# Kernel optimization log

Hardware: AMD Instinct MI355X
Metric: run time of the kernel (lower is better)

The kernel has to match this reference:

```python
import jax, jax.numpy as jnp
import numpy as np

H, W = 480, 640
OFFSETS = (1, 3, 5)
AXES = ('ud', 'lr', 'lu', 'ld')
EPS = 1e-18

def _xy_homo():
    yy, xx = jnp.meshgrid(jnp.arange(H, dtype=jnp.float32),
                          jnp.arange(W, dtype=jnp.float32), indexing='ij')
    return jnp.stack([xx.reshape(-1), yy.reshape(-1),
                      jnp.ones(H * W, jnp.float32)], 0)  # [3, H*W]

def _denom(normal, K_inv, xyh, dx, dy):
    # plane-induced denominator with pixel grid shifted by (dx, dy)
    b, _, h, w = normal.shape
    off = jnp.array([dx, dy, 0.0], jnp.float32)[:, None]
    p = jnp.matmul(K_inv, xyh + off).reshape(b, 3, h, w)
    return jnp.sum(normal * p, axis=1, keepdims=True)

def _shift_zero(t, o, axis):
    # zero-filled shifted copies per the torch cat patterns (conf / rgb)
    b, c, h, w = t.shape
    z = lambda *s: jnp.zeros((b, c) + s, t.dtype)
    cat = jnp.concatenate
    if axis == 'ud':
        return (cat([z(o, w), t[:, :, :-o, :]], 2),
                cat([t[:, :, o:, :], z(o, w)], 2))
    if axis == 'lr':
        return (cat([z(h, o), t[:, :, :, :-o]], 3),
                cat([t[:, :, :, o:], z(h, o)], 3))
    if axis == 'lu':
        t1 = cat([z(o, w), cat([z(h - o, o), t[:, :, :-o, :-o]], 3)], 2)
        t2 = cat([cat([t[:, :, o:, o:], z(h - o, o)], 3), z(o, w)], 2)
        return t1, t2
    # ld
    t1 = cat([cat([z(o, w - o), t[:, :, :-o, o:]], 2), z(h, o)], 3)
    t2 = cat([z(h, o), cat([t[:, :, o:, :-o], z(o, w - o)], 2)], 3)
    return t1, t2

def _propagate_axis(depth, normal, rgb, conf, o, K_inv, xyh, nom, axis):
    cat = jnp.concatenate
    def dprop(dx, dy):
        den = _denom(normal, K_inv, xyh, dx, dy)
        return jnp.clip(nom / (den + EPS), 0.01, 10.0)
    if axis == 'ud':
        d1 = cat([depth[:, :, :o, :], dprop(0, o)[:, :, :-o, :]], 2)
        d2 = cat([dprop(0, -o)[:, :, o:, :], depth[:, :, -o:, :]], 2)
    elif axis == 'lr':
        d1 = cat([depth[:, :, :, :o], dprop(o, 0)[:, :, :, :-o]], 3)
        d2 = cat([dprop(-o, 0)[:, :, :, o:], depth[:, :, :, -o:]], 3)
    elif axis == 'lu':
        d1t = cat([depth[:, :, o:, :o], dprop(o, o)[:, :, :-o, :-o]], 3)
        d1 = cat([depth[:, :, :o, :], d1t], 2)
        d2t = cat([dprop(-o, -o)[:, :, o:, o:], depth[:, :, :-o, -o:]], 3)
        d2 = cat([d2t, depth[:, :, -o:, :]], 2)
    else:  # 'ld'
        d1t = cat([depth[:, :, :o, :-o], dprop(-o, o)[:, :, :-o, o:]], 2)
        d1 = cat([d1t, depth[:, :, :, -o:]], 3)
        d2t = cat([dprop(o, -o)[:, :, o:, :-o], depth[:, :, -o:, :-o]], 2)
        d2 = cat([depth[:, :, :, :o], d2t], 3)
    conf1, conf2 = _shift_zero(conf, o, axis)
    rgb1, rgb2 = _shift_zero(rgb, o, axis)
    return d1, d2, conf1, conf2, rgb1, rgb2

def setup_inputs() -> dict:
    key = jax.random.key(0)
    k1, k2, k3, k4 = jax.random.split(key, 4)
    b = 2
    depth = jax.random.uniform(k1, (b, 1, H, W)) * 5.0 + 0.5
    n = jax.random.normal(k2, (b, 3, H, W))
    normal = n / (jnp.linalg.norm(n, axis=1, keepdims=True) + 1e-8)
    rgb = jax.random.uniform(k3, (b, 3, H, W))
    conf = jax.random.uniform(k4, (b, 1, H, W))
    K = np.array([[525.0, 0.0, W / 2.0], [0.0, 525.0, H / 2.0], [0.0, 0.0, 1.0]], np.float32)
    K_inv = jnp.broadcast_to(jnp.asarray(np.linalg.inv(K)), (b, 3, 3))
    return dict(depth=depth, normal=normal, rgb=rgb, conf=conf, K_inv=K_inv)

def reference(depth, normal, rgb, conf, K_inv):
    b, _, h, w = depth.shape
    xyh = _xy_homo()                                   # [3, H*W]
    xy3d = jnp.matmul(K_inv, xyh).reshape(b, 3, h, w)  # back-projected ray dirs
    nom = depth * jnp.sum(normal * xy3d, axis=1, keepdims=True)
    pd, pc, pr = [], [], []
    for o in OFFSETS:
        for axis in AXES:
            d1, d2, c1, c2, r1, r2 = _propagate_axis(depth, normal, rgb, conf, o, K_inv, xyh, nom, axis)
            pd += [d1, d2]; pc += [c1, c2]; pr += [r1, r2]
    pd = jnp.stack(pd, 1)  # [b, 24, 1, h, w]
    pc = jnp.stack(pc, 1)  # [b, 24, 1, h, w]
    pr = jnp.stack(pr, 1)  # [b, 24, 3, h, w]
    # pack propagated depth / conf / rgb along channel dim -> [b, 24, 5, h, w]
    return jnp.concatenate([pd, pc, pr], axis=2)
```

## Files before the change

### kernel.cpp

```cpp
#include <hip/hip_runtime.h>

static constexpr int IH = 480;
static constexpr int IW = 640;
static constexpr int IHW = IH * IW;

__device__ __constant__ const int c_oy[8] = { -1, +1,  0,  0, -1, +1, -1, +1 };
__device__ __constant__ const int c_ox[8] = {  0,  0, -1, +1, -1, +1, +1, -1 };

__global__ __launch_bounds__(256) void prop_kernel(
    const float* __restrict__ depth,
    const float* __restrict__ normal,
    const float* __restrict__ rgb,
    const float* __restrict__ conf,
    const float* __restrict__ Kinv,
    float* __restrict__ out)
{
    const int c  = blockIdx.y;
    const int bi = blockIdx.z;
    const int p  = blockIdx.x * 256 + threadIdx.x;
    const int y  = p / IW;
    const int x  = p - y * IW;

    const int oi = c >> 3;
    const int k  = c & 7;
    const int o  = 2 * oi + 1;
    const int oy = c_oy[k] * o;
    const int ox = c_ox[k] * o;

    const float* Ki = Kinv + bi * 9;
    const float k00 = Ki[0], k01 = Ki[1], k02 = Ki[2];
    const float k10 = Ki[3], k11 = Ki[4], k12 = Ki[5];
    const float k20 = Ki[6], k21 = Ki[7], k22 = Ki[8];

    const float fx = (float)x, fy = (float)y;
    const float r0 = k00 * fx + k01 * fy + k02;
    const float r1 = k10 * fx + k11 * fy + k12;
    const float r2 = k20 * fx + k21 * fy + k22;
    const float fox = (float)ox, foy = (float)oy;
    const float e0 = fox * k00 + foy * k01;
    const float e1 = fox * k10 + foy * k11;
    const float e2 = fox * k20 + foy * k21;

    const float* dp = depth  + (size_t)bi * IHW;
    const float* cf = conf   + (size_t)bi * IHW;
    const float* nr = normal + (size_t)bi * 3 * IHW;
    const float* rg = rgb    + (size_t)bi * 3 * IHW;

    const int sy = y + oy;
    const int sx = x + ox;

    float od, oc, og0, og1, og2;
    const bool inb = (sx >= 0) & (sx < IW) & (sy >= 0) & (sy < IH);
    if (inb) {
        const int sp = sy * IW + sx;
        const float n0 = nr[sp];
        const float n1 = nr[IHW + sp];
        const float n2 = nr[2 * IHW + sp];
        const float ds = dp[sp];
        oc  = cf[sp];
        og0 = rg[sp];
        og1 = rg[IHW + sp];
        og2 = rg[2 * IHW + sp];

        const float den = n0 * r0 + n1 * r1 + n2 * r2;
        const float t   = den + n0 * e0 + n1 * e1 + n2 * e2;
        const float v   = ds * t * __builtin_amdgcn_rcpf(den + 1e-18f);
        od = fminf(fmaxf(v, 0.01f), 10.0f);
    } else {
        if (k == 7 && sx >= 0 && sy >= IH) od = dp[y * IW + sx];
        else                               od = dp[p];
        oc = 0.0f; og0 = 0.0f; og1 = 0.0f; og2 = 0.0f;
    }

    float* ob = out + (((size_t)bi * 24 + c) * 5) * IHW + p;
    __builtin_nontemporal_store(od,  ob);
    __builtin_nontemporal_store(oc,  ob + IHW);
    __builtin_nontemporal_store(og0, ob + 2 * IHW);
    __builtin_nontemporal_store(og1, ob + 3 * IHW);
    __builtin_nontemporal_store(og2, ob + 4 * IHW);
}

extern "C" void kernel_launch(void* const* d_in, const int* in_sizes, int n_in,
                              void* d_out, int out_size, void* d_ws, size_t ws_size,
                              hipStream_t stream) {
    const float* depth  = (const float*)d_in[0];
    const float* normal = (const float*)d_in[1];
    const float* rgb    = (const float*)d_in[2];
    const float* conf   = (const float*)d_in[3];
    const float* Kinv   = (const float*)d_in[4];
    float* out = (float*)d_out;

    const int B = in_sizes[0] / IHW;
    dim3 grid(IHW / 256, 24, B);
    dim3 block(256, 1, 1);

    hipLaunchKernelGGL(prop_kernel, grid, block, 0, stream,
                       depth, normal, rgb, conf, Kinv, out);
}
```

Measured before the change: 75.21 us.

## Vectorize to 4 pixels per thread and split output channels across grid

```diff
diff --git a/kernel.cpp b/kernel.cpp
--- a/kernel.cpp
+++ b/kernel.cpp
@@ -3,6 +3,9 @@
 static constexpr int IH = 480;
 static constexpr int IW = 640;
 static constexpr int IHW = IH * IW;
+
+typedef float f32x4  __attribute__((ext_vector_type(4)));
+typedef float f32x4u __attribute__((ext_vector_type(4), aligned(4)));
 
 __device__ __constant__ const int c_oy[8] = { -1, +1,  0,  0, -1, +1, -1, +1 };
 __device__ __constant__ const int c_ox[8] = {  0,  0, -1, +1, -1, +1, +1, -1 };
@@ -15,69 +18,107 @@
     const float* __restrict__ Kinv,
     float* __restrict__ out)
 {
-    const int c  = blockIdx.y;
+    const int q  = blockIdx.y;
     const int bi = blockIdx.z;
-    const int p  = blockIdx.x * 256 + threadIdx.x;
-    const int y  = p / IW;
-    const int x  = p - y * IW;
-
+    const int c  = q / 5;
+    const int ch = q - c * 5;
     const int oi = c >> 3;
     const int k  = c & 7;
     const int o  = 2 * oi + 1;
     const int oy = c_oy[k] * o;
     const int ox = c_ox[k] * o;
 
+    const int p0 = (blockIdx.x * 256 + threadIdx.x) * 4;
+    const int y  = p0 / IW;
+    const int x0 = p0 - y * IW;
+    const int sy = y + oy;
+
+    const bool rowin   = (sy >= 0) & (sy < IH);
+    const bool fullcol = (x0 + ox >= 0) & (x0 + 3 + ox < IW);
+
+    float* ob = out + (((size_t)bi * 24 + c) * 5 + ch) * IHW + p0;
+
+    if (ch != 0) {
+        const float* sp = (ch == 1) ? (conf + (size_t)bi * IHW)
+                                    : (rgb + ((size_t)bi * 3 + (ch - 2)) * IHW);
+        f32x4 v;
+        if (rowin & fullcol) {
+            v = *reinterpret_cast<const f32x4u*>(sp + sy * IW + x0 + ox);
+        } else if (rowin) {
+#pragma unroll
+            for (int i = 0; i < 4; ++i) {
+                const int sx = x0 + i + ox;
+                v[i] = (sx >= 0 && sx < IW) ? sp[sy * IW + sx] : 0.0f;
+            }
+        } else {
+            v = (f32x4)0.0f;
+        }
+        __builtin_nontemporal_store(v, reinterpret_cast<f32x4*>(ob));
+        return;
+    }
+
+    const float* dp = depth  + (size_t)bi * IHW;
+    const float* nr = normal + (size_t)bi * 3 * IHW;
+
     const float* Ki = Kinv + bi * 9;
     const float k00 = Ki[0], k01 = Ki[1], k02 = Ki[2];
     const float k10 = Ki[3], k11 = Ki[4], k12 = Ki[5];
     const float k20 = Ki[6], k21 = Ki[7], k22 = Ki[8];
 
-    const float fx = (float)x, fy = (float)y;
-    const float r0 = k00 * fx + k01 * fy + k02;
-    const float r1 = k10 * fx + k11 * fy + k12;
-    const float r2 = k20 * fx + k21 * fy + k22;
+    const float fy  = (float)y;
     const float fox = (float)ox, foy = (float)oy;
-    const float e0 = fox * k00 + foy * k01;
-    const float e1 = fox * k10 + foy * k11;
-    const float e2 = fox * k20 + foy * k21;
+    const float e0  = fox * k00 + foy * k01;
+    const float e1  = fox * k10 + foy * k11;
+    const float e2  = fox * k20 + foy * k21;
 
-    const float* dp = depth  + (size_t)bi * IHW;
-    const float* cf = conf   + (size_t)bi * IHW;
-    const float* nr = normal + (size_t)bi * 3 * IHW;
-    const float* rg = rgb    + (size_t)bi * 3 * IHW;
-
-    const int sy = y + oy;
-    const int sx = x + ox;
-
-    float od, oc, og0, og1, og2;
-    const bool inb = (sx >= 0) & (sx < IW) & (sy >= 0) & (sy < IH);
-    if (inb) {
-        const int sp = sy * IW + sx;
-        const float n0 = nr[sp];
-        const float n1 = nr[IHW + sp];
-        const float n2 = nr[2 * IHW + sp];
-        const float ds = dp[sp];
-        oc  = cf[sp];
-        og0 = rg[sp];
-        og1 = rg[IHW + sp];
-        og2 = rg[2 * IHW + sp];
-
-        const float den = n0 * r0 + n1 * r1 + n2 * r2;
-        const float t   = den + n0 * e0 + n1 * e1 + n2 * e2;
-        const float v   = ds * t * __builtin_amdgcn_rcpf(den + 1e-18f);
-        od = fminf(fmaxf(v, 0.01f), 10.0f);
+    f32x4 v;
+    if (rowin & fullcol) {
+        const int spi = sy * IW + x0 + ox;
+        const f32x4 ds = *reinterpret_cast<const f32x4u*>(dp + spi);
+        const f32x4 n0 = *reinterpret_cast<const f32x4u*>(nr + spi);
+        const f32x4 n1 = *reinterpret_cast<const f32x4u*>(nr + IHW + spi);
+        const f32x4 n2 = *reinterpret_cast<const f32x4u*>(nr + 2 * IHW + spi);
+#pragma unroll
+        for (int i = 0; i < 4; ++i) {
+            const float fx = (float)(x0 + i);
+            const float r0 = k00 * fx + k01 * fy + k02;
+            const float r1 = k10 * fx + k11 * fy + k12;
+            const float r2 = k20 * fx + k21 * fy + k22;
+            const float den = n0[i] * r0 + n1[i] * r1 + n2[i] * r2;
+            const float t   = den + n0[i] * e0 + n1[i] * e1 + n2[i] * e2;
+            const float w   = ds[i] * t * __builtin_amdgcn_rcpf(den + 1e-18f);
+            v[i] = fminf(fmaxf(w, 0.01f), 10.0f);
+        }
+    } else if (rowin) {
+#pragma unroll
+        for (int i = 0; i < 4; ++i) {
+            const int sx = x0 + i + ox;
+            if (sx >= 0 && sx < IW) {
+                const int sp = sy * IW + sx;
+                const float n0 = nr[sp];
+                const float n1 = nr[IHW + sp];
+                const float n2 = nr[2 * IHW + sp];
+                const float fx = (float)(x0 + i);
+                const float r0 = k00 * fx + k01 * fy + k02;
+                const float r1 = k10 * fx + k11 * fy + k12;
+                const float r2 = k20 * fx + k21 * fy + k22;
+                const float den = n0 * r0 + n1 * r1 + n2 * r2;
+                const float t   = den + n0 * e0 + n1 * e1 + n2 * e2;
+                const float w   = dp[sp] * t * __builtin_amdgcn_rcpf(den + 1e-18f);
+                v[i] = fminf(fmaxf(w, 0.01f), 10.0f);
+            } else {
+                v[i] = dp[p0 + i];
+            }
+        }
     } else {
-        if (k == 7 && sx >= 0 && sy >= IH) od = dp[y * IW + sx];
-        else                               od = dp[p];
-        oc = 0.0f; og0 = 0.0f; og1 = 0.0f; og2 = 0.0f;
+#pragma unroll
+        for (int i = 0; i < 4; ++i) {
+            const int sx = x0 + i + ox;
+            if (k == 7 && sy >= IH && sx >= 0) v[i] = dp[y * IW + sx];
+            else                               v[i] = dp[p0 + i];
+        }
     }
-
-    float* ob = out + (((size_t)bi * 24 + c) * 5) * IHW + p;
-    __builtin_nontemporal_store(od,  ob);
-    __builtin_nontemporal_store(oc,  ob + IHW);
-    __builtin_nontemporal_store(og0, ob + 2 * IHW);
-    __builtin_nontemporal_store(og1, ob + 3 * IHW);
-    __builtin_nontemporal_store(og2, ob + 4 * IHW);
+    __builtin_nontemporal_store(v, reinterpret_cast<f32x4*>(ob));
 }
 
 extern "C" void kernel_launch(void* const* d_in, const int* in_sizes, int n_in,
@@ -91,7 +132,7 @@
     float* out = (float*)d_out;
 
     const int B = in_sizes[0] / IHW;
-    dim3 grid(IHW / 256, 24, B);
+    dim3 grid(IHW / (256 * 4), 120, B);
     dim3 block(256, 1, 1);
 
     hipLaunchKernelGGL(prop_kernel, grid, block, 0, stream,
```

Measured after the change: 92.96 us. +23.6%, slower.
